# Kernel tuning notes

Hardware: AMD Instinct MI355X
Metric: run time of the kernel (lower is better)

Reference implementation:

```python
import jax, jax.numpy as jnp
import numpy as np

Q = 127.0  # int8 absmax quantization denominator


def _make_quant_weight(key, out_dim, in_dim):
    """Emulate bitsandbytes Linear8bitLt weight: int8 matrix + per-row absmax scale."""
    k1, k2 = jax.random.split(key)
    w_fp = jax.random.normal(k1, (out_dim, in_dim), dtype=jnp.float32) * 0.02
    scale = jnp.max(jnp.abs(w_fp), axis=1)  # [out_dim] per-row absmax
    w_int8 = jnp.clip(jnp.round(w_fp / scale[:, None] * Q), -127, 127).astype(jnp.int8)
    return w_int8, scale


def setup_inputs() -> dict:
    key = jax.random.key(0)
    ks = jax.random.split(key, 4)
    B, S, H, I = 4, 1024, 5120, 12288
    x = jax.random.normal(ks[0], (B, S, H), dtype=jnp.float32)
    w_gate, s_gate = _make_quant_weight(ks[1], I, H)
    w_up, s_up = _make_quant_weight(ks[2], I, H)
    w_down, s_down = _make_quant_weight(ks[3], H, I)
    return {"x": x, "w_gate": w_gate, "s_gate": s_gate,
            "w_up": w_up, "s_up": s_up,
            "w_down": w_down, "s_down": s_down}


def _qlinear(x, w_int8, scale):
    # y = x @ dequant(W)^T ; dequant(W) = w_int8 * scale/127 per output row.
    # Fold scale after the matmul (equivalent, avoids materializing dequant W twice).
    y = jnp.einsum("bsh,oh->bso", x, w_int8.astype(x.dtype))
    return y * (scale / Q)


def reference(x, w_gate, s_gate, w_up, s_up, w_down, s_down):
    gate = jax.nn.silu(_qlinear(x, w_gate, s_gate))  # [B,S,I]
    up = _qlinear(x, w_up, s_up)                     # [B,S,I]
    return _qlinear(gate * up, w_down, s_down)       # [B,S,H]
```

## Files before the change

kernel.cpp:

```cpp
#include <hip/hip_runtime.h>
#include <hip/hip_bf16.h>
#include <stdint.h>

typedef unsigned short u16;
typedef __attribute__((ext_vector_type(4))) float floatx4;
typedef __attribute__((ext_vector_type(8))) short bf16x8;
typedef const __attribute__((address_space(1))) void gvoid;
typedef __attribute__((address_space(3))) void lvoid;

static constexpr int Mdim = 4096;
static constexpr int Hdim = 5120;
static constexpr int Idim = 12288;
static constexpr float QINV = 1.0f / 127.0f;

__global__ void conv_i32_to_bf16(const int* __restrict__ in, u16* __restrict__ out) {
    int idx = (blockIdx.x * 256 + threadIdx.x) * 4;
    int4 v = *(const int4*)(in + idx);
    __hip_bfloat16 b0 = __float2bfloat16((float)v.x);
    __hip_bfloat16 b1 = __float2bfloat16((float)v.y);
    __hip_bfloat16 b2 = __float2bfloat16((float)v.z);
    __hip_bfloat16 b3 = __float2bfloat16((float)v.w);
    ushort4 o;
    o.x = *(u16*)&b0; o.y = *(u16*)&b1; o.z = *(u16*)&b2; o.w = *(u16*)&b3;
    *(ushort4*)(out + idx) = o;
}

__global__ void conv_f32_to_bf16(const float* __restrict__ in, u16* __restrict__ out) {
    int idx = (blockIdx.x * 256 + threadIdx.x) * 4;
    float4 v = *(const float4*)(in + idx);
    __hip_bfloat16 b0 = __float2bfloat16(v.x);
    __hip_bfloat16 b1 = __float2bfloat16(v.y);
    __hip_bfloat16 b2 = __float2bfloat16(v.z);
    __hip_bfloat16 b3 = __float2bfloat16(v.w);
    ushort4 o;
    o.x = *(u16*)&b0; o.y = *(u16*)&b1; o.z = *(u16*)&b2; o.w = *(u16*)&b3;
    *(ushort4*)(out + idx) = o;
}

template<int MODE>
__global__ __launch_bounds__(256)
void gemm_bt(const u16* __restrict__ A, const u16* __restrict__ Bw,
             const float* __restrict__ scale, u16* __restrict__ GateBuf,
             float* __restrict__ OutF, int N, int K)
{
    constexpr int BM = 128, BN = 128, BK = 64;
    __shared__ u16 As[BM * BK];
    __shared__ u16 Bs[BN * BK];
    const int tid  = threadIdx.x;
    const int lane = tid & 63;
    const int wave = tid >> 6;
    const int row0 = blockIdx.x * BM;
    const int col0 = blockIdx.y * BN;
    const int wm = (wave & 1) * 64;
    const int wn = (wave >> 1) * 64;
    const int lm = lane & 15;
    const int lg = lane >> 4;

    floatx4 acc[4][4];
    #pragma unroll
    for (int i = 0; i < 4; i++)
        #pragma unroll
        for (int j = 0; j < 4; j++)
            acc[i][j] = (floatx4){0.f, 0.f, 0.f, 0.f};

    const u16* Ablk = A  + (size_t)row0 * K;
    const u16* Bblk = Bw + (size_t)col0 * K;

    for (int kt = 0; kt < K; kt += BK) {
        __syncthreads();
        #pragma unroll
        for (int i = 0; i < 4; i++) {
            int slot = i * 256 + tid;
            int r = slot >> 3;
            int u = slot & 7;
            int c = (u ^ (r & 7)) * 8;
            __builtin_amdgcn_global_load_lds((gvoid*)(Ablk + (size_t)r * K + kt + c),
                                             (lvoid*)(As + slot * 8), 16, 0, 0);
            __builtin_amdgcn_global_load_lds((gvoid*)(Bblk + (size_t)r * K + kt + c),
                                             (lvoid*)(Bs + slot * 8), 16, 0, 0);
        }
        __syncthreads();
        #pragma unroll
        for (int kk = 0; kk < BK; kk += 32) {
            bf16x8 af[4], bfr[4];
            #pragma unroll
            for (int i = 0; i < 4; i++) {
                const int rA = wm + i * 16 + lm;
                const int rB = wn + i * 16 + lm;
                const int uu = ((kk >> 3) + lg);
                af[i]  = *(const bf16x8*)(As + rA * BK + ((uu ^ (lm & 7)) << 3));
                bfr[i] = *(const bf16x8*)(Bs + rB * BK + ((uu ^ (lm & 7)) << 3));
            }
            #pragma unroll
            for (int i = 0; i < 4; i++)
                #pragma unroll
                for (int j = 0; j < 4; j++)
                    acc[i][j] = __builtin_amdgcn_mfma_f32_16x16x32_bf16(af[i], bfr[j], acc[i][j], 0, 0, 0);
        }
    }

    const int ln = lane & 15;
    const int rq = (lane >> 4) * 4;
    #pragma unroll
    for (int j = 0; j < 4; j++) {
        const int col = col0 + wn + j * 16 + ln;
        const float s = scale[col] * QINV;
        #pragma unroll
        for (int i = 0; i < 4; i++) {
            const int rowb = row0 + wm + i * 16 + rq;
            #pragma unroll
            for (int r = 0; r < 4; r++) {
                const size_t idx = (size_t)(rowb + r) * N + col;
                float v = acc[i][j][r] * s;
                if (MODE == 0) {
                    float g = v / (1.0f + __expf(-v));
                    __hip_bfloat16 h = __float2bfloat16(g);
                    GateBuf[idx] = *(u16*)&h;
                } else if (MODE == 1) {
                    u16 gu = GateBuf[idx];
                    float g = __bfloat162float(*(__hip_bfloat16*)&gu);
                    __hip_bfloat16 h = __float2bfloat16(g * v);
                    GateBuf[idx] = *(u16*)&h;
                } else {
                    OutF[idx] = v;
                }
            }
        }
    }
}

extern "C" void kernel_launch(void* const* d_in, const int* in_sizes, int n_in,
                              void* d_out, int out_size, void* d_ws, size_t ws_size,
                              hipStream_t stream)
{
    const float* x  = (const float*)d_in[0];
    const int*   wg = (const int*)d_in[1];
    const float* sg = (const float*)d_in[2];
    const int*   wu = (const int*)d_in[3];
    const float* su = (const float*)d_in[4];
    const int*   wd = (const int*)d_in[5];
    const float* sd = (const float*)d_in[6];
    float* out = (float*)d_out;

    char* ws = (char*)d_ws;
    u16* xb   = (u16*)ws;
    u16* wb   = (u16*)(ws + 41943040);
    u16* gate = (u16*)(ws + 41943040 + 125829120);

    conv_f32_to_bf16<<<20480, 256, 0, stream>>>(x, xb);

    conv_i32_to_bf16<<<61440, 256, 0, stream>>>(wg, wb);
    gemm_bt<0><<<dim3(Mdim / 128, Idim / 128), 256, 0, stream>>>(xb, wb, sg, gate, nullptr, Idim, Hdim);

    conv_i32_to_bf16<<<61440, 256, 0, stream>>>(wu, wb);
    gemm_bt<1><<<dim3(Mdim / 128, Idim / 128), 256, 0, stream>>>(xb, wb, su, gate, nullptr, Idim, Hdim);

    conv_i32_to_bf16<<<61440, 256, 0, stream>>>(wd, wb);
    gemm_bt<2><<<dim3(Mdim / 128, Hdim / 128), 256, 0, stream>>>(gate, wb, sd, nullptr, out, Hdim, Idim);
}
```

Measured before the change: 2.934 ms.

## Use 256x256 tiles with a 4-stage async LDS pipeline and block swizzle

Replaces the 128x128, 256-thread GEMM with a 256x256, 512-thread kernel. It keeps a 4-deep ring of BK=32 LDS buffers fed by global_load_lds, with split A/B staging phases, waitcnt-based barriers and setprio around the MFMA bursts. It also adds an XCD-aware block swizzle and widens the conversion kernels to 8 elements per thread. The goals are hiding global-load latency, raising arithmetic intensity per tile and improving L2 locality. The cost is more registers (128 accumulator floats per lane) and 128KB of LDS per block, which may limit occupancy.

```diff
diff --git a/kernel.cpp b/kernel.cpp
--- a/kernel.cpp
+++ b/kernel.cpp
@@ -5,6 +5,7 @@
 typedef unsigned short u16;
 typedef __attribute__((ext_vector_type(4))) float floatx4;
 typedef __attribute__((ext_vector_type(8))) short bf16x8;
+typedef __attribute__((ext_vector_type(8))) unsigned short u16x8;
 typedef const __attribute__((address_space(1))) void gvoid;
 typedef __attribute__((address_space(3))) void lvoid;
 
@@ -13,91 +14,150 @@
 static constexpr int Idim = 12288;
 static constexpr float QINV = 1.0f / 127.0f;
 
+static __device__ __forceinline__ u16 f2b(float f) {
+    __hip_bfloat16 h = __float2bfloat16(f);
+    return *(u16*)&h;
+}
+
 __global__ void conv_i32_to_bf16(const int* __restrict__ in, u16* __restrict__ out) {
-    int idx = (blockIdx.x * 256 + threadIdx.x) * 4;
-    int4 v = *(const int4*)(in + idx);
-    __hip_bfloat16 b0 = __float2bfloat16((float)v.x);
-    __hip_bfloat16 b1 = __float2bfloat16((float)v.y);
-    __hip_bfloat16 b2 = __float2bfloat16((float)v.z);
-    __hip_bfloat16 b3 = __float2bfloat16((float)v.w);
-    ushort4 o;
-    o.x = *(u16*)&b0; o.y = *(u16*)&b1; o.z = *(u16*)&b2; o.w = *(u16*)&b3;
-    *(ushort4*)(out + idx) = o;
+    int idx = (blockIdx.x * 256 + threadIdx.x) * 8;
+    int4 v0 = *(const int4*)(in + idx);
+    int4 v1 = *(const int4*)(in + idx + 4);
+    u16x8 o;
+    o[0] = f2b((float)v0.x); o[1] = f2b((float)v0.y);
+    o[2] = f2b((float)v0.z); o[3] = f2b((float)v0.w);
+    o[4] = f2b((float)v1.x); o[5] = f2b((float)v1.y);
+    o[6] = f2b((float)v1.z); o[7] = f2b((float)v1.w);
+    *(u16x8*)(out + idx) = o;
 }
 
 __global__ void conv_f32_to_bf16(const float* __restrict__ in, u16* __restrict__ out) {
-    int idx = (blockIdx.x * 256 + threadIdx.x) * 4;
-    float4 v = *(const float4*)(in + idx);
-    __hip_bfloat16 b0 = __float2bfloat16(v.x);
-    __hip_bfloat16 b1 = __float2bfloat16(v.y);
-    __hip_bfloat16 b2 = __float2bfloat16(v.z);
-    __hip_bfloat16 b3 = __float2bfloat16(v.w);
-    ushort4 o;
-    o.x = *(u16*)&b0; o.y = *(u16*)&b1; o.z = *(u16*)&b2; o.w = *(u16*)&b3;
-    *(ushort4*)(out + idx) = o;
+    int idx = (blockIdx.x * 256 + threadIdx.x) * 8;
+    float4 v0 = *(const float4*)(in + idx);
+    float4 v1 = *(const float4*)(in + idx + 4);
+    u16x8 o;
+    o[0] = f2b(v0.x); o[1] = f2b(v0.y); o[2] = f2b(v0.z); o[3] = f2b(v0.w);
+    o[4] = f2b(v1.x); o[5] = f2b(v1.y); o[6] = f2b(v1.z); o[7] = f2b(v1.w);
+    *(u16x8*)(out + idx) = o;
 }
 
 template<int MODE>
-__global__ __launch_bounds__(256)
-void gemm_bt(const u16* __restrict__ A, const u16* __restrict__ Bw,
+__global__ __launch_bounds__(512, 2)
+void gemm256(const u16* __restrict__ A, const u16* __restrict__ Bw,
              const float* __restrict__ scale, u16* __restrict__ GateBuf,
-             float* __restrict__ OutF, int N, int K)
+             float* __restrict__ OutF, int N, int K, int nbx)
 {
-    constexpr int BM = 128, BN = 128, BK = 64;
-    __shared__ u16 As[BM * BK];
-    __shared__ u16 Bs[BN * BK];
+    __shared__ u16 As[4 * 8192];
+    __shared__ u16 Bs[4 * 8192];
+
     const int tid  = threadIdx.x;
     const int lane = tid & 63;
     const int wave = tid >> 6;
-    const int row0 = blockIdx.x * BM;
-    const int col0 = blockIdx.y * BN;
-    const int wm = (wave & 1) * 64;
-    const int wn = (wave >> 1) * 64;
+    const int wm = (wave >> 2) * 128;
+    const int wn = (wave & 3) * 64;
     const int lm = lane & 15;
     const int lg = lane >> 4;
 
-    floatx4 acc[4][4];
+    const int nwg = gridDim.x;
+    const int bid = blockIdx.x;
+    const int swz = (bid & 7) * (nwg >> 3) + (bid >> 3);
+    const int row0 = (swz % nbx) * 256;
+    const int col0 = (swz / nbx) * 256;
+
+    const u16* Ablk = A  + (size_t)row0 * K;
+    const u16* Bblk = Bw + (size_t)col0 * K;
+
+    const int rs  = tid >> 2;
+    const int csw = ((tid & 3) ^ ((rs >> 1) & 3)) << 3;
+    const u16* aS = Ablk + (size_t)rs * K + csw;
+    const u16* bS = Bblk + (size_t)rs * K + csw;
+    const size_t rK128 = (size_t)128 * K;
+    u16* aD = As + tid * 8;
+    u16* bD = Bs + tid * 8;
+
+    const int koff = (lg ^ ((lm >> 1) & 3)) << 3;
+
+    floatx4 acc[8][4];
     #pragma unroll
-    for (int i = 0; i < 4; i++)
+    for (int i = 0; i < 8; i++)
         #pragma unroll
         for (int j = 0; j < 4; j++)
             acc[i][j] = (floatx4){0.f, 0.f, 0.f, 0.f};
 
-    const u16* Ablk = A  + (size_t)row0 * K;
-    const u16* Bblk = Bw + (size_t)col0 * K;
-
-    for (int kt = 0; kt < K; kt += BK) {
-        __syncthreads();
-        #pragma unroll
-        for (int i = 0; i < 4; i++) {
-            int slot = i * 256 + tid;
-            int r = slot >> 3;
-            int u = slot & 7;
-            int c = (u ^ (r & 7)) * 8;
-            __builtin_amdgcn_global_load_lds((gvoid*)(Ablk + (size_t)r * K + kt + c),
-                                             (lvoid*)(As + slot * 8), 16, 0, 0);
-            __builtin_amdgcn_global_load_lds((gvoid*)(Bblk + (size_t)r * K + kt + c),
-                                             (lvoid*)(Bs + slot * 8), 16, 0, 0);
-        }
-        __syncthreads();
-        #pragma unroll
-        for (int kk = 0; kk < BK; kk += 32) {
-            bf16x8 af[4], bfr[4];
-            #pragma unroll
-            for (int i = 0; i < 4; i++) {
-                const int rA = wm + i * 16 + lm;
-                const int rB = wn + i * 16 + lm;
-                const int uu = ((kk >> 3) + lg);
-                af[i]  = *(const bf16x8*)(As + rA * BK + ((uu ^ (lm & 7)) << 3));
-                bfr[i] = *(const bf16x8*)(Bs + rB * BK + ((uu ^ (lm & 7)) << 3));
-            }
-            #pragma unroll
-            for (int i = 0; i < 4; i++)
-                #pragma unroll
-                for (int j = 0; j < 4; j++)
-                    acc[i][j] = __builtin_amdgcn_mfma_f32_16x16x32_bf16(af[i], bfr[j], acc[i][j], 0, 0, 0);
-        }
-    }
+    const int nt = K >> 5;
+
+#define STAGE_A(t) do { \
+    const u16* s_ = aS + (size_t)(t) * 32; \
+    u16* d_ = aD + ((t) & 3) * 8192; \
+    __builtin_amdgcn_global_load_lds((gvoid*)s_, (lvoid*)d_, 16, 0, 0); \
+    __builtin_amdgcn_global_load_lds((gvoid*)(s_ + rK128), (lvoid*)(d_ + 4096), 16, 0, 0); \
+} while (0)
+
+#define STAGE_B(t) do { \
+    const u16* s_ = bS + (size_t)(t) * 32; \
+    u16* d_ = bD + ((t) & 3) * 8192; \
+    __builtin_amdgcn_global_load_lds((gvoid*)s_, (lvoid*)d_, 16, 0, 0); \
+    __builtin_amdgcn_global_load_lds((gvoid*)(s_ + rK128), (lvoid*)(d_ + 4096), 16, 0, 0); \
+} while (0)
+
+#define PHASE(qr, STG, WAITV) do { \
+    bf16x8 af[4], bf[4]; \
+    const u16* Ab_ = As + bufo; \
+    const u16* Bb_ = Bs + bufo; \
+    _Pragma("unroll") \
+    for (int i = 0; i < 4; i++) \
+        af[i] = *(const bf16x8*)(Ab_ + (wm + ((qr) * 4 + i) * 16 + lm) * 32 + koff); \
+    _Pragma("unroll") \
+    for (int j = 0; j < 4; j++) \
+        bf[j] = *(const bf16x8*)(Bb_ + (wn + j * 16 + lm) * 32 + koff); \
+    STG; \
+    asm volatile("" ::: "memory"); \
+    __builtin_amdgcn_s_barrier(); \
+    __builtin_amdgcn_s_setprio(1); \
+    _Pragma("unroll") \
+    for (int i = 0; i < 4; i++) \
+        _Pragma("unroll") \
+        for (int j = 0; j < 4; j++) \
+            acc[(qr) * 4 + i][j] = __builtin_amdgcn_mfma_f32_16x16x32_bf16( \
+                af[i], bf[j], acc[(qr) * 4 + i][j], 0, 0, 0); \
+    __builtin_amdgcn_s_setprio(0); \
+    WAITV; \
+    asm volatile("" ::: "memory"); \
+    __builtin_amdgcn_s_barrier(); \
+} while (0)
+
+    STAGE_A(0); STAGE_B(0);
+    STAGE_A(1); STAGE_B(1);
+    STAGE_A(2); STAGE_B(2);
+    asm volatile("s_waitcnt vmcnt(8)" ::: "memory");
+    __builtin_amdgcn_s_barrier();
+
+    int t = 0;
+    for (; t < nt - 3; ++t) {
+        const int bufo = (t & 3) * 8192;
+        PHASE(0, STAGE_A(t + 3), (void)0);
+        PHASE(1, STAGE_B(t + 3), asm volatile("s_waitcnt vmcnt(8)" ::: "memory"));
+    }
+    {
+        const int bufo = (t & 3) * 8192;
+        PHASE(0, (void)0, (void)0);
+        PHASE(1, (void)0, asm volatile("s_waitcnt vmcnt(4)" ::: "memory"));
+        ++t;
+    }
+    {
+        const int bufo = (t & 3) * 8192;
+        PHASE(0, (void)0, (void)0);
+        PHASE(1, (void)0, asm volatile("s_waitcnt vmcnt(0)" ::: "memory"));
+        ++t;
+    }
+    {
+        const int bufo = (t & 3) * 8192;
+        PHASE(0, (void)0, (void)0);
+        PHASE(1, (void)0, (void)0);
+    }
+#undef PHASE
+#undef STAGE_A
+#undef STAGE_B
 
     const int ln = lane & 15;
     const int rq = (lane >> 4) * 4;
@@ -106,7 +166,7 @@
         const int col = col0 + wn + j * 16 + ln;
         const float s = scale[col] * QINV;
         #pragma unroll
-        for (int i = 0; i < 4; i++) {
+        for (int i = 0; i < 8; i++) {
             const int rowb = row0 + wm + i * 16 + rq;
             #pragma unroll
             for (int r = 0; r < 4; r++) {
@@ -114,13 +174,11 @@
                 float v = acc[i][j][r] * s;
                 if (MODE == 0) {
                     float g = v / (1.0f + __expf(-v));
-                    __hip_bfloat16 h = __float2bfloat16(g);
-                    GateBuf[idx] = *(u16*)&h;
+                    GateBuf[idx] = f2b(g);
                 } else if (MODE == 1) {
                     u16 gu = GateBuf[idx];
                     float g = __bfloat162float(*(__hip_bfloat16*)&gu);
-                    __hip_bfloat16 h = __float2bfloat16(g * v);
-                    GateBuf[idx] = *(u16*)&h;
+                    GateBuf[idx] = f2b(g * v);
                 } else {
                     OutF[idx] = v;
                 }
@@ -147,14 +205,17 @@
     u16* wb   = (u16*)(ws + 41943040);
     u16* gate = (u16*)(ws + 41943040 + 125829120);
 
-    conv_f32_to_bf16<<<20480, 256, 0, stream>>>(x, xb);
-
-    conv_i32_to_bf16<<<61440, 256, 0, stream>>>(wg, wb);
-    gemm_bt<0><<<dim3(Mdim / 128, Idim / 128), 256, 0, stream>>>(xb, wb, sg, gate, nullptr, Idim, Hdim);
-
-    conv_i32_to_bf16<<<61440, 256, 0, stream>>>(wu, wb);
-    gemm_bt<1><<<dim3(Mdim / 128, Idim / 128), 256, 0, stream>>>(xb, wb, su, gate, nullptr, Idim, Hdim);
-
-    conv_i32_to_bf16<<<61440, 256, 0, stream>>>(wd, wb);
-    gemm_bt<2><<<dim3(Mdim / 128, Hdim / 128), 256, 0, stream>>>(gate, wb, sd, nullptr, out, Hdim, Idim);
-}
+    conv_f32_to_bf16<<<10240, 256, 0, stream>>>(x, xb);
+
+    conv_i32_to_bf16<<<30720, 256, 0, stream>>>(wg, wb);
+    gemm256<0><<<(Mdim / 256) * (Idim / 256), 512, 0, stream>>>(
+        xb, wb, sg, gate, nullptr, Idim, Hdim, Mdim / 256);
+
+    conv_i32_to_bf16<<<30720, 256, 0, stream>>>(wu, wb);
+    gemm256<1><<<(Mdim / 256) * (Idim / 256), 512, 0, stream>>>(
+        xb, wb, su, gate, nullptr, Idim, Hdim, Mdim / 256);
+
+    conv_i32_to_bf16<<<30720, 256, 0, stream>>>(wd, wb);
+    gemm256<2><<<(Mdim / 256) * (Hdim / 256), 512, 0, stream>>>(
+        gate, wb, sd, nullptr, out, Hdim, Idim, Mdim / 256);
+}
```

Result: faster. 2.581 ms (-12.0%).
